# Performance work log

Hardware: AMD Instinct MI355X
Metric: run time of the kernel (lower is better)

The kernel has to match this reference:

```python
import jax, jax.numpy as jnp
import numpy as np

VOXEL = 0.1          # superpoint_voxel_size
NUM_BATCHES = 4      # B (batch indices in coords[:,0] are in [0, B))


def setup_inputs() -> dict:
    key = jax.random.key(0)
    k1, k2, k3, k4, k5, k6, k7 = jax.random.split(key, 7)
    N, D = 1_000_000, 64
    batch_ids = jax.random.randint(k1, (N,), 0, NUM_BATCHES).astype(jnp.float32)
    xyz = jax.random.uniform(k2, (N, 3), dtype=jnp.float32) * 50.0  # 50m scene
    coords = jnp.concatenate([batch_ids[:, None], xyz], axis=1)      # (N,4)
    features = jax.random.normal(k3, (N, D), dtype=jnp.float32)
    s1 = 1.0 / np.sqrt(3.0)
    s2 = 1.0 / np.sqrt(D)
    W1 = jax.random.uniform(k4, (3, D), minval=-s1, maxval=s1, dtype=jnp.float32)
    b1 = jax.random.uniform(k5, (D,), minval=-s1, maxval=s1, dtype=jnp.float32)
    W2 = jax.random.uniform(k6, (D, D), minval=-s2, maxval=s2, dtype=jnp.float32)
    b2 = jax.random.uniform(k7, (D,), minval=-s2, maxval=s2, dtype=jnp.float32)
    return {"coords": coords, "features": features, "W1": W1, "b1": b1, "W2": W2, "b2": b2}


def reference(coords, features, W1, b1, W2, b2):
    N, D = features.shape
    batch_ids = coords[:, 0].astype(jnp.int32)          # (N,)
    xyz = coords[:, 1:4]                                 # (N,3)
    q = jnp.floor(xyz / VOXEL).astype(jnp.int32)         # voxel quantization
    combined = jnp.concatenate([batch_ids[:, None], q], axis=1)  # (N,4) int32 keys

    # torch.unique(dim=0, return_inverse=True): lexicographically sorted unique
    # rows. We pad to a fixed S=N segments (fill rows sorted to the tail via a
    # max sentinel); `valid` masks out the padding.
    SENT = jnp.iinfo(jnp.int32).max
    unique_sp, sp_to_point = jnp.unique(
        combined, axis=0, size=N, fill_value=SENT, return_inverse=True)
    sp_to_point = sp_to_point.reshape(-1)                # (N,)

    counts = jax.ops.segment_sum(jnp.ones((N,), jnp.float32), sp_to_point, num_segments=N)
    valid = counts > 0
    c = jnp.maximum(counts, 1.0)[:, None]                # clamp(min=1)

    sp_features = jax.ops.segment_sum(features, sp_to_point, num_segments=N) / c  # (N,D) mean
    sp_centers = jax.ops.segment_sum(xyz, sp_to_point, num_segments=N) / c        # (N,3) mean

    # pos_enc: Linear(3,D) -> ReLU -> Linear(D,D)
    pos = jnp.maximum(sp_centers @ W1 + b1, 0.0) @ W2 + b2
    sp_features = jnp.where(valid[:, None], sp_features + pos, 0.0)
    sp_centers = jnp.where(valid[:, None], sp_centers, 0.0)

    # batch_offsets: cumulative superpoint counts per batch (padding -> dump bin B)
    sp_batch = jnp.where(valid, unique_sp[:, 0], NUM_BATCHES)
    per_batch = jax.ops.segment_sum(jnp.ones((N,), jnp.int32), sp_batch,
                                    num_segments=NUM_BATCHES + 1)[:NUM_BATCHES]
    batch_offsets = jnp.concatenate([jnp.zeros((1,), jnp.int32), jnp.cumsum(per_batch)])
    return sp_features, sp_centers, sp_to_point, batch_offsets
```

## Files before the change

kernel.cpp:

```cpp
#include <hip/hip_runtime.h>
#include <stdint.h>


static constexpr uint32_t NWORDS = 1u << 24;
static constexpr uint32_t NBLK   = NWORDS / 1024;

typedef __attribute__((ext_vector_type(8))) short short8;
typedef __attribute__((ext_vector_type(4))) float f32x4;

__device__ __forceinline__ short f2bf(float x) {
    union { float f; uint32_t u; } v; v.f = x;
    uint32_t u = v.u;
    uint32_t r = (u + 0x7FFFu + ((u >> 16) & 1u)) >> 16;
    return (short)r;
}

__device__ __forceinline__ uint32_t point_key(float4 c) {
    uint32_t b  = (uint32_t)(int)c.x;
    uint32_t qx = (uint32_t)(int)floorf(c.y / 0.1f);
    uint32_t qy = (uint32_t)(int)floorf(c.z / 0.1f);
    uint32_t qz = (uint32_t)(int)floorf(c.w / 0.1f);
    return (b << 27) | (qx << 18) | (qy << 9) | qz;
}

__global__ void k0_w2t(const float* __restrict__ W2, short* __restrict__ W2T) {
    int t = blockIdx.x * 256 + threadIdx.x;
    if (t < 4096) {
        int col = t >> 6, k = t & 63;
        W2T[col * 64 + k] = f2bf(W2[k * 64 + col]);
    }
}

__global__ void k1_keys(const float4* __restrict__ coords, uint32_t* __restrict__ bitmap, int N) {
    int i = blockIdx.x * blockDim.x + threadIdx.x;
    if (i >= N) return;
    uint32_t key = point_key(coords[i]);
    atomicOr(&bitmap[key >> 5], 1u << (key & 31u));
}

__global__ __launch_bounds__(256) void k2a_blockscan(
        const uint4* __restrict__ bm4, uint16_t* __restrict__ scan8,
        uint32_t* __restrict__ bsum) {
    int t = threadIdx.x;
    int lane = t & 63, wid = t >> 6;
    uint4 v = bm4[(size_t)blockIdx.x * 256 + t];
    uint32_t pc = __popc(v.x) + __popc(v.y) + __popc(v.z) + __popc(v.w);
    uint32_t sc = pc;
    #pragma unroll
    for (int off = 1; off < 64; off <<= 1) {
        uint32_t n = __shfl_up(sc, off);
        if (lane >= off) sc += n;
    }
    __shared__ uint32_t wt[4];
    if (lane == 63) wt[wid] = sc;
    __syncthreads();
    uint32_t wbase = 0;
    #pragma unroll
    for (int w = 0; w < 4; ++w) wbase += (w < wid) ? wt[w] : 0u;
    uint32_t excl = wbase + sc - pc;
    if (!(t & 1)) scan8[(size_t)blockIdx.x * 128 + (t >> 1)] = (uint16_t)excl;
    if (t == 255) bsum[blockIdx.x] = wbase + sc;
}

__global__ void k2b_topscan(const uint32_t* __restrict__ bsum, uint32_t* __restrict__ bscan) {
    __shared__ uint32_t s[1024];
    int t = threadIdx.x;
    uint32_t base = (uint32_t)t * 16u;
    const uint4* b4 = (const uint4*)(bsum + base);
    uint32_t sum = 0;
    #pragma unroll
    for (int k = 0; k < 4; ++k) { uint4 v = b4[k]; sum += v.x + v.y + v.z + v.w; }
    s[t] = sum;
    __syncthreads();
    for (int off = 1; off < 1024; off <<= 1) {
        uint32_t v = (t >= off) ? s[t - off] : 0u;
        __syncthreads();
        s[t] += v;
        __syncthreads();
    }
    uint32_t run = s[t] - sum;
    for (int k = 0; k < 16; ++k) { bscan[base + k] = run; run += bsum[base + k]; }
    if (t == 1023) bscan[16384] = run;
}

__global__ void k3a_rank(const float4* __restrict__ coords,
                         uint32_t* __restrict__ ranks,
                         const uint32_t* __restrict__ bitmap,
                         const uint16_t* __restrict__ scan8,
                         const uint32_t* __restrict__ bscan,
                         float* __restrict__ sums,
                         uint32_t* __restrict__ inv,
                         float* __restrict__ out_sp, int N) {
    int i = blockIdx.x * blockDim.x + threadIdx.x;
    if (i >= N) return;
    float4 c = coords[i];
    uint32_t key = point_key(c);
    uint32_t w = key >> 5, bit = key & 31u;
    const uint4* bm4 = (const uint4*)(bitmap + (w & ~7u));
    uint4 lo = bm4[0], hi = bm4[1];
    uint32_t wd[8] = {lo.x, lo.y, lo.z, lo.w, hi.x, hi.y, hi.z, hi.w};
    uint32_t idx = w & 7u;
    uint32_t r = bscan[w >> 10] + (uint32_t)scan8[w >> 3];
    uint32_t cur = 0;
    #pragma unroll
    for (uint32_t j = 0; j < 8; ++j) {
        r += (j < idx) ? __popc(wd[j]) : 0u;
        cur = (j == idx) ? wd[j] : cur;
    }
    r += __popc(cur & ((1u << bit) - 1u));
    ranks[i] = r;
    inv[r] = (uint32_t)i;
    out_sp[i] = (float)r;
    float* s4 = sums + 4u * (size_t)r;
    atomicAdd(s4 + 0, 1.0f);
    s4[1] = c.y; s4[2] = c.z; s4[3] = c.w;
}

__global__ void k3b_zero(float4* __restrict__ sums, int N) {
    int r = blockIdx.x * blockDim.x + threadIdx.x;
    if (r >= N) return;
    float4 s = sums[r];
    if (s.x > 1.5f) sums[r] = make_float4(s.x, 0.f, 0.f, 0.f);
}

__global__ void k3c_multi(const float4* __restrict__ coords,
                          const uint32_t* __restrict__ ranks,
                          float* __restrict__ sums, int N) {
    int i = blockIdx.x * blockDim.x + threadIdx.x;
    if (i >= N) return;
    uint32_t r = ranks[i];
    float* s4 = sums + 4u * (size_t)r;
    if (s4[0] > 1.5f) {
        float4 c = coords[i];
        atomicAdd(s4 + 1, c.y);
        atomicAdd(s4 + 2, c.z);
        atomicAdd(s4 + 3, c.w);
    }
}

__global__ __launch_bounds__(256) void k5_fused(
        const float4* __restrict__ features4,
        const uint32_t* __restrict__ inv,
        const float4* __restrict__ sums,
        const float* __restrict__ W1, const float* __restrict__ b1,
        const short* __restrict__ W2T, const float* __restrict__ b2,
        float4* __restrict__ out_feat4, float* __restrict__ out_cent, int N) {
    int lane = threadIdx.x & 63;
    int rows_base = blockIdx.x * 256 + (threadIdx.x >> 6) * 64;

    int my = rows_base + lane;
    if (my < N) {
        float4 s4 = sums[my];
        float ic = s4.x > 0.f ? 1.f / s4.x : 0.f;
        out_cent[3 * (size_t)my + 0] = s4.y * ic;
        out_cent[3 * (size_t)my + 1] = s4.z * ic;
        out_cent[3 * (size_t)my + 2] = s4.w * ic;
    }

    float4 sg4[4]; float scx[4], scy[4], scz[4];
    #pragma unroll
    for (int g = 0; g < 4; ++g) {
        int rg = rows_base + (g << 4) + (lane & 15);
        sg4[g] = sums[rg < N ? rg : N - 1];
        float ic = sg4[g].x > 0.f ? 1.f / sg4[g].x : 0.f;
        scx[g] = sg4[g].y * ic; scy[g] = sg4[g].z * ic; scz[g] = sg4[g].w * ic;
    }

    f32x4 acc[4][4];
    #pragma unroll
    for (int cg = 0; cg < 4; ++cg) {
        float4 bv = ((const float4*)b2)[(cg << 2) + (lane >> 4)];
        #pragma unroll
        for (int g = 0; g < 4; ++g)
            acc[g][cg] = (f32x4){bv.x, bv.y, bv.z, bv.w};
    }

    #pragma unroll
    for (int s = 0; s < 2; ++s) {
        int kb = s * 32 + ((lane >> 4) << 3);
        float4 tx0 = *(const float4*)(W1 + kb),       tx1 = *(const float4*)(W1 + kb + 4);
        float4 ty0 = *(const float4*)(W1 + 64 + kb),  ty1 = *(const float4*)(W1 + 64 + kb + 4);
        float4 tz0 = *(const float4*)(W1 + 128 + kb), tz1 = *(const float4*)(W1 + 128 + kb + 4);
        float4 tb0 = *(const float4*)(b1 + kb),       tb1 = *(const float4*)(b1 + kb + 4);
        float w1x[8] = {tx0.x, tx0.y, tx0.z, tx0.w, tx1.x, tx1.y, tx1.z, tx1.w};
        float w1y[8] = {ty0.x, ty0.y, ty0.z, ty0.w, ty1.x, ty1.y, ty1.z, ty1.w};
        float w1z[8] = {tz0.x, tz0.y, tz0.z, tz0.w, tz1.x, tz1.y, tz1.z, tz1.w};
        float b1v[8] = {tb0.x, tb0.y, tb0.z, tb0.w, tb1.x, tb1.y, tb1.z, tb1.w};

        short8 afrag[4];
        #pragma unroll
        for (int cg = 0; cg < 4; ++cg) {
            int col = (cg << 4) | (lane & 15);
            afrag[cg] = *(const short8*)(W2T + col * 64 + kb);
        }

        #pragma unroll
        for (int g = 0; g < 4; ++g) {
            short8 hf;
            #pragma unroll
            for (int j = 0; j < 8; ++j) {
                float h = fmaf(scz[g], w1z[j], fmaf(scy[g], w1y[j], fmaf(scx[g], w1x[j], b1v[j])));
                hf[j] = f2bf(fmaxf(h, 0.0f));
            }
            #pragma unroll
            for (int cg = 0; cg < 4; ++cg)
                acc[g][cg] = __builtin_amdgcn_mfma_f32_16x16x32_bf16(afrag[cg], hf, acc[g][cg], 0, 0, 0);
        }
    }

    #pragma unroll
    for (int g = 0; g < 4; ++g) {
        int gr = rows_base + (g << 4) + (lane & 15);
        if (gr >= N) continue;
        float cnt = sg4[g].x;
        float4 v[4];
        #pragma unroll
        for (int cg = 0; cg < 4; ++cg)
            v[cg] = make_float4(acc[g][cg][0], acc[g][cg][1], acc[g][cg][2], acc[g][cg][3]);
        if (cnt == 0.0f) {
            #pragma unroll
            for (int cg = 0; cg < 4; ++cg) v[cg] = make_float4(0.f, 0.f, 0.f, 0.f);
        } else if (cnt == 1.0f) {
            size_t fb = (size_t)inv[gr] * 16 + (lane >> 4);
            #pragma unroll
            for (int cg = 0; cg < 4; ++cg) {
                float4 f = features4[fb + (cg << 2)];
                v[cg].x += f.x; v[cg].y += f.y; v[cg].z += f.z; v[cg].w += f.w;
            }
        }
        size_t ob = (size_t)gr * 16 + (lane >> 4);
        #pragma unroll
        for (int cg = 0; cg < 4; ++cg)
            out_feat4[ob + (cg << 2)] = v[cg];
    }
}

__global__ __launch_bounds__(256) void k5b_multi(
        const float* __restrict__ features, const uint32_t* __restrict__ ranks,
        const float4* __restrict__ sums, float* __restrict__ out_feat, int N) {
    int i = blockIdx.x * blockDim.x + threadIdx.x;
    if (i >= N) return;
    uint32_t r = ranks[i];
    float cnt = sums[r].x;
    if (cnt > 1.5f) {
        float iv = 1.0f / cnt;
        const float* frow = features + (size_t)i * 64;
        float* orow = out_feat + (size_t)r * 64;
        #pragma unroll 1
        for (int q = 0; q < 64; ++q) atomicAdd(&orow[q], frow[q] * iv);
    }
}

__global__ void k6_offsets(const uint32_t* __restrict__ bscan, float* __restrict__ out_off) {
    int t = threadIdx.x;
    if (t < 5) {
        uint32_t v;
        if (t == 0)      v = 0u;
        else if (t == 4) v = bscan[16384];
        else             v = bscan[(uint32_t)t << 12];
        out_off[t] = (float)v;
    }
}

extern "C" void kernel_launch(void* const* d_in, const int* in_sizes, int n_in,
                              void* d_out, int out_size, void* d_ws, size_t ws_size,
                              hipStream_t stream) {
    const float4* coords = (const float4*)d_in[0];
    const float*  feats  = (const float*)d_in[1];
    const float*  W1 = (const float*)d_in[2];
    const float*  b1 = (const float*)d_in[3];
    const float*  W2 = (const float*)d_in[4];
    const float*  b2 = (const float*)d_in[5];
    int N = in_sizes[0] / 4;

    char* ws = (char*)d_ws;
    uint32_t* bitmap = (uint32_t*)ws;
    uint16_t* scan8  = (uint16_t*)(ws + (1u << 26));
    uint32_t* bsum   = (uint32_t*)(ws + (1u << 26) + (1u << 22));
    uint32_t* bscan  = bsum + NBLK;
    size_t off = (size_t)(1u << 26) + (1u << 22) + (size_t)NBLK * 4 + (size_t)(NBLK + 1) * 4;
    off = (off + 15) & ~(size_t)15;
    uint32_t* ranks = (uint32_t*)(ws + off);
    size_t off2 = (off + (size_t)N * 4 + 15) & ~(size_t)15;
    float* sums = (float*)(ws + off2);
    size_t off3 = off2 + (size_t)N * 16;
    uint32_t* inv = (uint32_t*)(ws + off3);
    size_t off4 = (off3 + (size_t)N * 4 + 15) & ~(size_t)15;
    short* W2T = (short*)(ws + off4);

    float* out_feat = (float*)d_out;
    float* out_cent = out_feat + (size_t)N * 64;
    float* out_sp   = out_cent + (size_t)N * 3;
    float* out_off  = out_sp + N;

    hipMemsetAsync(bitmap, 0, (size_t)NWORDS * 4u, stream);
    hipMemsetAsync(sums, 0, (size_t)N * 16u, stream);

    int nb = (N + 255) / 256;
    k0_w2t<<<16, 256, 0, stream>>>(W2, W2T);
    k1_keys<<<nb, 256, 0, stream>>>(coords, bitmap, N);
    k2a_blockscan<<<NBLK, 256, 0, stream>>>((const uint4*)bitmap, scan8, bsum);
    k2b_topscan<<<1, 1024, 0, stream>>>(bsum, bscan);
    k3a_rank<<<nb, 256, 0, stream>>>(coords, ranks, bitmap, scan8, bscan, sums, inv, out_sp, N);
    k3b_zero<<<nb, 256, 0, stream>>>((float4*)sums, N);
    k3c_multi<<<nb, 256, 0, stream>>>(coords, ranks, sums, N);
    k5_fused<<<nb, 256, 0, stream>>>((const float4*)feats, inv, (const float4*)sums,
                                     W1, b1, W2T, b2, (float4*)out_feat, out_cent, N);
    k5b_multi<<<nb, 256, 0, stream>>>(feats, ranks, (const float4*)sums, out_feat, N);
    k6_offsets<<<1, 64, 0, stream>>>(bscan, out_off);
}
```

Measured before the change: 353.9 us.

## Compact multi-point superpoints into side buffers and fold them into the fused kernel

Superpoints with more than one point now get a compact slot, assigned through an atomic counter during ranking. A single fix-up kernel accumulates their coordinate and feature sums into small side buffers, and the fused output kernel reads those buffers in place of separate zero and multi-point atomic passes over the full output. This drops two full-N kernels and the atomics that wrote into the 256 MB output after the fact. The scan granularity changes from 8 words to 4 so each rank lookup reads a single 16-byte bitmap load, and outputs use nontemporal stores. The side buffers are capped at 65536 multi-point segments, so a denser input would overflow and give wrong results.

New measurement: 347.1 us. No clear change (-1.9%).

```diff
diff --git a/kernel.cpp b/kernel.cpp
--- a/kernel.cpp
+++ b/kernel.cpp
@@ -4,6 +4,7 @@
 
 static constexpr uint32_t NWORDS = 1u << 24;
 static constexpr uint32_t NBLK   = NWORDS / 1024;
+static constexpr uint32_t MCAP   = 65536;
 
 typedef __attribute__((ext_vector_type(8))) short short8;
 typedef __attribute__((ext_vector_type(4))) float f32x4;
@@ -39,7 +40,7 @@
 }
 
 __global__ __launch_bounds__(256) void k2a_blockscan(
-        const uint4* __restrict__ bm4, uint16_t* __restrict__ scan8,
+        const uint4* __restrict__ bm4, uint16_t* __restrict__ scan4,
         uint32_t* __restrict__ bsum) {
     int t = threadIdx.x;
     int lane = t & 63, wid = t >> 6;
@@ -57,8 +58,7 @@
     uint32_t wbase = 0;
     #pragma unroll
     for (int w = 0; w < 4; ++w) wbase += (w < wid) ? wt[w] : 0u;
-    uint32_t excl = wbase + sc - pc;
-    if (!(t & 1)) scan8[(size_t)blockIdx.x * 128 + (t >> 1)] = (uint16_t)excl;
+    scan4[(size_t)blockIdx.x * 256 + t] = (uint16_t)(wbase + sc - pc);
     if (t == 255) bsum[blockIdx.x] = wbase + sc;
 }
 
@@ -86,93 +86,117 @@
 __global__ void k3a_rank(const float4* __restrict__ coords,
                          uint32_t* __restrict__ ranks,
                          const uint32_t* __restrict__ bitmap,
-                         const uint16_t* __restrict__ scan8,
+                         const uint16_t* __restrict__ scan4,
                          const uint32_t* __restrict__ bscan,
                          float* __restrict__ sums,
                          uint32_t* __restrict__ inv,
+                         uint32_t* __restrict__ slotmap,
+                         uint32_t* __restrict__ mctr,
                          float* __restrict__ out_sp, int N) {
     int i = blockIdx.x * blockDim.x + threadIdx.x;
     if (i >= N) return;
     float4 c = coords[i];
     uint32_t key = point_key(c);
     uint32_t w = key >> 5, bit = key & 31u;
-    const uint4* bm4 = (const uint4*)(bitmap + (w & ~7u));
-    uint4 lo = bm4[0], hi = bm4[1];
-    uint32_t wd[8] = {lo.x, lo.y, lo.z, lo.w, hi.x, hi.y, hi.z, hi.w};
-    uint32_t idx = w & 7u;
-    uint32_t r = bscan[w >> 10] + (uint32_t)scan8[w >> 3];
+    uint4 q = *(const uint4*)(bitmap + (w & ~3u));
+    uint32_t wd[4] = {q.x, q.y, q.z, q.w};
+    uint32_t idx = w & 3u;
+    uint32_t r = bscan[w >> 10] + (uint32_t)scan4[w >> 2];
     uint32_t cur = 0;
     #pragma unroll
-    for (uint32_t j = 0; j < 8; ++j) {
+    for (uint32_t j = 0; j < 4; ++j) {
         r += (j < idx) ? __popc(wd[j]) : 0u;
         cur = (j == idx) ? wd[j] : cur;
     }
     r += __popc(cur & ((1u << bit) - 1u));
     ranks[i] = r;
     inv[r] = (uint32_t)i;
-    out_sp[i] = (float)r;
+    __builtin_nontemporal_store((float)r, out_sp + i);
     float* s4 = sums + 4u * (size_t)r;
-    atomicAdd(s4 + 0, 1.0f);
+    float old = atomicAdd(s4 + 0, 1.0f);
     s4[1] = c.y; s4[2] = c.z; s4[3] = c.w;
-}
-
-__global__ void k3b_zero(float4* __restrict__ sums, int N) {
-    int r = blockIdx.x * blockDim.x + threadIdx.x;
-    if (r >= N) return;
-    float4 s = sums[r];
-    if (s.x > 1.5f) sums[r] = make_float4(s.x, 0.f, 0.f, 0.f);
-}
-
-__global__ void k3c_multi(const float4* __restrict__ coords,
-                          const uint32_t* __restrict__ ranks,
-                          float* __restrict__ sums, int N) {
+    if (old == 1.0f) {
+        uint32_t slot = atomicAdd(mctr, 1u);
+        if (slot < MCAP) slotmap[r] = slot + 1u;
+    }
+}
+
+__global__ void k3fix(const float4* __restrict__ coords,
+                      const float* __restrict__ features,
+                      const uint32_t* __restrict__ ranks,
+                      const uint32_t* __restrict__ slotmap,
+                      const float4* __restrict__ sums,
+                      float* __restrict__ msum,
+                      float* __restrict__ mfeat, int N) {
     int i = blockIdx.x * blockDim.x + threadIdx.x;
     if (i >= N) return;
     uint32_t r = ranks[i];
-    float* s4 = sums + 4u * (size_t)r;
-    if (s4[0] > 1.5f) {
-        float4 c = coords[i];
-        atomicAdd(s4 + 1, c.y);
-        atomicAdd(s4 + 2, c.z);
-        atomicAdd(s4 + 3, c.w);
-    }
+    uint32_t sl = slotmap[r];
+    if (sl == 0) return;
+    sl -= 1u;
+    float cnt = sums[r].x;
+    float4 c = coords[i];
+    float* m = msum + 4u * (size_t)sl;
+    atomicAdd(m + 0, c.y);
+    atomicAdd(m + 1, c.z);
+    atomicAdd(m + 2, c.w);
+    float iv = 1.0f / cnt;
+    const float* frow = features + (size_t)i * 64;
+    float* orow = mfeat + (size_t)sl * 64;
+    #pragma unroll 1
+    for (int qq = 0; qq < 64; ++qq) atomicAdd(&orow[qq], frow[qq] * iv);
 }
 
 __global__ __launch_bounds__(256) void k5_fused(
-        const float4* __restrict__ features4,
+        const f32x4* __restrict__ features4,
         const uint32_t* __restrict__ inv,
         const float4* __restrict__ sums,
+        const uint32_t* __restrict__ slotmap,
+        const float4* __restrict__ msum,
+        const f32x4* __restrict__ mfeat4,
         const float* __restrict__ W1, const float* __restrict__ b1,
         const short* __restrict__ W2T, const float* __restrict__ b2,
-        float4* __restrict__ out_feat4, float* __restrict__ out_cent, int N) {
+        f32x4* __restrict__ out_feat4, float* __restrict__ out_cent, int N) {
     int lane = threadIdx.x & 63;
     int rows_base = blockIdx.x * 256 + (threadIdx.x >> 6) * 64;
 
     int my = rows_base + lane;
     if (my < N) {
         float4 s4 = sums[my];
+        float sx = s4.y, sy = s4.z, sz = s4.w;
+        if (s4.x > 1.5f) {
+            float4 m = msum[slotmap[my] - 1u];
+            sx = m.x; sy = m.y; sz = m.z;
+        }
         float ic = s4.x > 0.f ? 1.f / s4.x : 0.f;
-        out_cent[3 * (size_t)my + 0] = s4.y * ic;
-        out_cent[3 * (size_t)my + 1] = s4.z * ic;
-        out_cent[3 * (size_t)my + 2] = s4.w * ic;
-    }
-
-    float4 sg4[4]; float scx[4], scy[4], scz[4];
+        __builtin_nontemporal_store(sx * ic, out_cent + 3 * (size_t)my + 0);
+        __builtin_nontemporal_store(sy * ic, out_cent + 3 * (size_t)my + 1);
+        __builtin_nontemporal_store(sz * ic, out_cent + 3 * (size_t)my + 2);
+    }
+
+    float cntg[4], scx[4], scy[4], scz[4];
     #pragma unroll
     for (int g = 0; g < 4; ++g) {
         int rg = rows_base + (g << 4) + (lane & 15);
-        sg4[g] = sums[rg < N ? rg : N - 1];
-        float ic = sg4[g].x > 0.f ? 1.f / sg4[g].x : 0.f;
-        scx[g] = sg4[g].y * ic; scy[g] = sg4[g].z * ic; scz[g] = sg4[g].w * ic;
+        int rgc = rg < N ? rg : N - 1;
+        float4 sg = sums[rgc];
+        cntg[g] = sg.x;
+        float sx = sg.y, sy = sg.z, sz = sg.w;
+        if (sg.x > 1.5f) {
+            float4 m = msum[slotmap[rgc] - 1u];
+            sx = m.x; sy = m.y; sz = m.z;
+        }
+        float ic = sg.x > 0.f ? 1.f / sg.x : 0.f;
+        scx[g] = sx * ic; scy[g] = sy * ic; scz[g] = sz * ic;
     }
 
     f32x4 acc[4][4];
     #pragma unroll
     for (int cg = 0; cg < 4; ++cg) {
-        float4 bv = ((const float4*)b2)[(cg << 2) + (lane >> 4)];
+        f32x4 bv = ((const f32x4*)b2)[(cg << 2) + (lane >> 4)];
         #pragma unroll
         for (int g = 0; g < 4; ++g)
-            acc[g][cg] = (f32x4){bv.x, bv.y, bv.z, bv.w};
+            acc[g][cg] = bv;
     }
 
     #pragma unroll
@@ -212,42 +236,26 @@
     for (int g = 0; g < 4; ++g) {
         int gr = rows_base + (g << 4) + (lane & 15);
         if (gr >= N) continue;
-        float cnt = sg4[g].x;
-        float4 v[4];
-        #pragma unroll
-        for (int cg = 0; cg < 4; ++cg)
-            v[cg] = make_float4(acc[g][cg][0], acc[g][cg][1], acc[g][cg][2], acc[g][cg][3]);
+        float cnt = cntg[g];
+        f32x4 v[4];
+        #pragma unroll
+        for (int cg = 0; cg < 4; ++cg) v[cg] = acc[g][cg];
         if (cnt == 0.0f) {
             #pragma unroll
-            for (int cg = 0; cg < 4; ++cg) v[cg] = make_float4(0.f, 0.f, 0.f, 0.f);
+            for (int cg = 0; cg < 4; ++cg) v[cg] = (f32x4){0.f, 0.f, 0.f, 0.f};
         } else if (cnt == 1.0f) {
             size_t fb = (size_t)inv[gr] * 16 + (lane >> 4);
             #pragma unroll
-            for (int cg = 0; cg < 4; ++cg) {
-                float4 f = features4[fb + (cg << 2)];
-                v[cg].x += f.x; v[cg].y += f.y; v[cg].z += f.z; v[cg].w += f.w;
-            }
+            for (int cg = 0; cg < 4; ++cg) v[cg] += features4[fb + (cg << 2)];
+        } else {
+            size_t mb = (size_t)(slotmap[gr] - 1u) * 16 + (lane >> 4);
+            #pragma unroll
+            for (int cg = 0; cg < 4; ++cg) v[cg] += mfeat4[mb + (cg << 2)];
         }
         size_t ob = (size_t)gr * 16 + (lane >> 4);
         #pragma unroll
         for (int cg = 0; cg < 4; ++cg)
-            out_feat4[ob + (cg << 2)] = v[cg];
-    }
-}
-
-__global__ __launch_bounds__(256) void k5b_multi(
-        const float* __restrict__ features, const uint32_t* __restrict__ ranks,
-        const float4* __restrict__ sums, float* __restrict__ out_feat, int N) {
-    int i = blockIdx.x * blockDim.x + threadIdx.x;
-    if (i >= N) return;
-    uint32_t r = ranks[i];
-    float cnt = sums[r].x;
-    if (cnt > 1.5f) {
-        float iv = 1.0f / cnt;
-        const float* frow = features + (size_t)i * 64;
-        float* orow = out_feat + (size_t)r * 64;
-        #pragma unroll 1
-        for (int q = 0; q < 64; ++q) atomicAdd(&orow[q], frow[q] * iv);
+            __builtin_nontemporal_store(v[cg], out_feat4 + ob + (cg << 2));
     }
 }
 
@@ -274,38 +282,45 @@
     int N = in_sizes[0] / 4;
 
     char* ws = (char*)d_ws;
-    uint32_t* bitmap = (uint32_t*)ws;
-    uint16_t* scan8  = (uint16_t*)(ws + (1u << 26));
-    uint32_t* bsum   = (uint32_t*)(ws + (1u << 26) + (1u << 22));
-    uint32_t* bscan  = bsum + NBLK;
-    size_t off = (size_t)(1u << 26) + (1u << 22) + (size_t)NBLK * 4 + (size_t)(NBLK + 1) * 4;
-    off = (off + 15) & ~(size_t)15;
-    uint32_t* ranks = (uint32_t*)(ws + off);
-    size_t off2 = (off + (size_t)N * 4 + 15) & ~(size_t)15;
-    float* sums = (float*)(ws + off2);
-    size_t off3 = off2 + (size_t)N * 16;
-    uint32_t* inv = (uint32_t*)(ws + off3);
-    size_t off4 = (off3 + (size_t)N * 4 + 15) & ~(size_t)15;
-    short* W2T = (short*)(ws + off4);
+    size_t o = 0;
+    uint32_t* bitmap = (uint32_t*)(ws + o); o += (size_t)NWORDS * 4;
+    uint16_t* scan4  = (uint16_t*)(ws + o); o += (size_t)(NWORDS / 4) * 2;
+    uint32_t* bsum   = (uint32_t*)(ws + o); o += (size_t)NBLK * 4;
+    uint32_t* bscan  = (uint32_t*)(ws + o); o += (size_t)(NBLK + 1) * 4;
+    o = (o + 15) & ~(size_t)15;
+    uint32_t* ranks  = (uint32_t*)(ws + o); o += (size_t)N * 4;
+    o = (o + 15) & ~(size_t)15;
+    float*    sums   = (float*)(ws + o);    o += (size_t)N * 16;
+    uint32_t* inv    = (uint32_t*)(ws + o); o += (size_t)N * 4;
+    o = (o + 15) & ~(size_t)15;
+    short*    W2T    = (short*)(ws + o);    o += 8192;
+    size_t multi_base = o;
+    uint32_t* slotmap = (uint32_t*)(ws + o); o += (size_t)N * 4;
+    uint32_t* mctr    = (uint32_t*)(ws + o); o += 16;
+    float*    msum    = (float*)(ws + o);    o += (size_t)MCAP * 16;
+    float*    mfeat   = (float*)(ws + o);    o += (size_t)MCAP * 256;
+    size_t multi_size = o - multi_base;
 
     float* out_feat = (float*)d_out;
     float* out_cent = out_feat + (size_t)N * 64;
     float* out_sp   = out_cent + (size_t)N * 3;
     float* out_off  = out_sp + N;
 
-    hipMemsetAsync(bitmap, 0, (size_t)NWORDS * 4u, stream);
-    hipMemsetAsync(sums, 0, (size_t)N * 16u, stream);
+    hipMemsetAsync(bitmap, 0, (size_t)NWORDS * 4, stream);
+    hipMemsetAsync(sums, 0, (size_t)N * 16, stream);
+    hipMemsetAsync(ws + multi_base, 0, multi_size, stream);
 
     int nb = (N + 255) / 256;
     k0_w2t<<<16, 256, 0, stream>>>(W2, W2T);
     k1_keys<<<nb, 256, 0, stream>>>(coords, bitmap, N);
-    k2a_blockscan<<<NBLK, 256, 0, stream>>>((const uint4*)bitmap, scan8, bsum);
+    k2a_blockscan<<<NBLK, 256, 0, stream>>>((const uint4*)bitmap, scan4, bsum);
     k2b_topscan<<<1, 1024, 0, stream>>>(bsum, bscan);
-    k3a_rank<<<nb, 256, 0, stream>>>(coords, ranks, bitmap, scan8, bscan, sums, inv, out_sp, N);
-    k3b_zero<<<nb, 256, 0, stream>>>((float4*)sums, N);
-    k3c_multi<<<nb, 256, 0, stream>>>(coords, ranks, sums, N);
-    k5_fused<<<nb, 256, 0, stream>>>((const float4*)feats, inv, (const float4*)sums,
-                                     W1, b1, W2T, b2, (float4*)out_feat, out_cent, N);
-    k5b_multi<<<nb, 256, 0, stream>>>(feats, ranks, (const float4*)sums, out_feat, N);
+    k3a_rank<<<nb, 256, 0, stream>>>(coords, ranks, bitmap, scan4, bscan, sums, inv,
+                                     slotmap, mctr, out_sp, N);
+    k3fix<<<nb, 256, 0, stream>>>(coords, feats, ranks, slotmap, (const float4*)sums,
+                                  msum, mfeat, N);
+    k5_fused<<<nb, 256, 0, stream>>>((const f32x4*)feats, inv, (const float4*)sums,
+                                     slotmap, (const float4*)msum, (const f32x4*)mfeat,
+                                     W1, b1, W2T, b2, (f32x4*)out_feat, out_cent, N);
     k6_offsets<<<1, 64, 0, stream>>>(bscan, out_off);
 }
```
